# Performance work log

Measured on AMD Instinct MI355X. Metric: run time of the kernel, lower is better.

Reference implementation:

```python
import jax, jax.numpy as jnp
import numpy as np

NG, G = 256, 32          # num groups, pedestrians per group
E, H, MID, BN_EPS = 64, 64, 512, 1e-5
BOT = 32

def _bn(x, gamma, beta):
    # training-mode BatchNorm1d applied PER GROUP (axis=1 are the rows of
    # that group's pairwise batch), biased variance, eps=1e-5
    mean = jnp.mean(x, axis=1, keepdims=True)
    var = jnp.mean((x - mean) ** 2, axis=1, keepdims=True)
    return gamma * (x - mean) * jax.lax.rsqrt(var + BN_EPS) + beta

def setup_inputs() -> dict:
    key = jax.random.key(0)
    ks = jax.random.split(key, 8)
    B = NG * G
    starts = np.arange(NG, dtype=np.int64) * G
    seq_start_end = jnp.asarray(np.stack([starts, starts + G], axis=1))
    def lin(k, fi, fo):
        kw, kb = jax.random.split(k)
        lim = 1.0 / np.sqrt(fi)
        return (jax.random.uniform(kw, (fi, fo), jnp.float32, -lim, lim),
                jax.random.uniform(kb, (fo,), jnp.float32, -lim, lim))
    W_spatial, b_spatial = lin(ks[0], 2, E)
    W1, b1 = lin(ks[1], E + H, MID)
    W2, b2 = lin(ks[2], MID, BOT)
    return {
        'h_states': jax.random.normal(ks[3], (1, B, H), jnp.float32),
        'seq_start_end': seq_start_end,
        'end_pos': jax.random.normal(ks[4], (B, 2), jnp.float32),
        'W_spatial': W_spatial, 'b_spatial': b_spatial,
        'W1': W1, 'b1': b1,
        'gamma1': jnp.ones((MID,), jnp.float32), 'beta1': jnp.zeros((MID,), jnp.float32),
        'W2': W2, 'b2': b2,
        'gamma2': jnp.ones((BOT,), jnp.float32), 'beta2': jnp.zeros((BOT,), jnp.float32),
    }

def reference(h_states, seq_start_end, end_pos, W_spatial, b_spatial,
              W1, b1, gamma1, beta1, W2, b2, gamma2, beta2):
    B = end_pos.shape[0]
    ng = seq_start_end.shape[0]
    g = B // ng  # equal-size groups -> fully vectorized
    h = h_states.reshape(B, H).reshape(ng, g, H)
    pos = end_pos.reshape(ng, g, 2)
    # rel[n, i, j] = pos[n, j] - pos[n, i]  (matches repeat/tile in torch code)
    rel = pos[:, None, :, :] - pos[:, :, None, :]            # (ng, g, g, 2)
    emb = rel @ W_spatial + b_spatial                         # (ng, g, g, E)
    hb = jnp.broadcast_to(h[:, None, :, :], (ng, g, g, H))    # hidden of ped j
    x = jnp.concatenate([emb, hb], axis=-1).reshape(ng, g * g, E + H)
    x = jax.nn.relu(_bn(x @ W1 + b1, gamma1, beta1))          # (ng, g*g, 512)
    x = jax.nn.relu(_bn(x @ W2 + b2, gamma2, beta2))          # (ng, g*g, 32)
    pool = x.reshape(ng, g, g, BOT).max(axis=2)               # max over j
    return pool.reshape(B, BOT)
```

## Files before the change

### kernel.cpp

```cpp
#include <hip/hip_runtime.h>

#define GRP 32
#define HD 64
#define MIDD 512
#define LDSTR 520

typedef _Float16 half8 __attribute__((ext_vector_type(8)));
typedef float floatx4 __attribute__((ext_vector_type(4)));

__device__ inline half8 relu8(half8 x) {
    return __builtin_elementwise_max(x, (half8)(_Float16)0);
}

__launch_bounds__(512, 2)
__global__ void pool_all(const float* __restrict__ h_states,
                         const float* __restrict__ end_pos,
                         const float* __restrict__ Ws,
                         const float* __restrict__ W1,
                         const float* __restrict__ gamma1,
                         const float* __restrict__ beta1,
                         const float* __restrict__ W2,
                         const float* __restrict__ gamma2,
                         const float* __restrict__ beta2,
                         float* __restrict__ out) {
    __shared__ _Float16 Ash[32][LDSTR];
    __shared__ _Float16 Bsh[32][LDSTR];
    __shared__ _Float16 w2T[32][LDSTR];
    __shared__ float posx[32], posy[32];
    __shared__ float wr0s[512], wr1s[512];
    __shared__ float red[8][2][16][2];
    __shared__ float bns[32], bno[32];

    const int tid  = threadIdx.x;
    const int wave = tid >> 6;
    const int lane = tid & 63;
    const int quad = lane >> 4;
    const int n16  = lane & 15;
    const int g0   = blockIdx.x * GRP;

    if (tid < 32) {
        posx[tid] = end_pos[(g0 + tid) * 2];
        posy[tid] = end_pos[(g0 + tid) * 2 + 1];
    }

    half8 afr[2][2];
#pragma unroll
    for (int mt = 0; mt < 2; ++mt)
#pragma unroll
        for (int kk = 0; kk < 2; ++kk) {
            const float4* hp = (const float4*)(h_states + (size_t)(g0 + mt * 16 + n16) * HD + kk * 32 + quad * 8);
            float4 p0 = hp[0], p1 = hp[1];
            half8 a;
            a[0] = (_Float16)p0.x; a[1] = (_Float16)p0.y; a[2] = (_Float16)p0.z; a[3] = (_Float16)p0.w;
            a[4] = (_Float16)p1.x; a[5] = (_Float16)p1.y; a[6] = (_Float16)p1.z; a[7] = (_Float16)p1.w;
            afr[mt][kk] = a;
        }

    {
        const int c = tid;
        float p0[4] = {0.f, 0.f, 0.f, 0.f}, p1[4] = {0.f, 0.f, 0.f, 0.f};
#pragma unroll
        for (int e = 0; e < 64; e += 4) {
#pragma unroll
            for (int u = 0; u < 4; ++u) {
                float w = W1[(e + u) * MIDD + c];
                p0[u] = fmaf(Ws[e + u], w, p0[u]);
                p1[u] = fmaf(Ws[64 + e + u], w, p1[u]);
            }
        }
        wr0s[c] = (p0[0] + p0[1]) + (p0[2] + p0[3]);
        wr1s[c] = (p1[0] + p1[1]) + (p1[2] + p1[3]);
    }

    {
        const float4* W2v = (const float4*)W2;
#pragma unroll
        for (int it = 0; it < 8; ++it) {
            int i4 = tid + it * 512;
            float4 p = W2v[i4];
            int k = i4 >> 3, nn = (i4 & 7) * 4;
            w2T[nn][k]     = (_Float16)p.x;
            w2T[nn + 1][k] = (_Float16)p.y;
            w2T[nn + 2][k] = (_Float16)p.z;
            w2T[nn + 3][k] = (_Float16)p.w;
        }
    }

    floatx4 acc[2][4];
#pragma unroll
    for (int a = 0; a < 2; ++a)
#pragma unroll
        for (int b = 0; b < 4; ++b) acc[a][b] = (floatx4){0.f, 0.f, 0.f, 0.f};

    half8 bfr[4][2];
#pragma unroll
    for (int nt4 = 0; nt4 < 4; ++nt4) {
        const int c = (wave * 4 + nt4) * 16 + n16;
#pragma unroll
        for (int kk = 0; kk < 2; ++kk) {
            float t[8];
#pragma unroll
            for (int x = 0; x < 8; ++x) {
                int k = kk * 32 + quad * 8 + x;
                t[x] = W1[(size_t)(64 + k) * MIDD + c];
            }
            half8 b;
#pragma unroll
            for (int x = 0; x < 8; ++x) b[x] = (_Float16)t[x];
            bfr[nt4][kk] = b;
        }
    }
#pragma unroll
    for (int nt4 = 0; nt4 < 4; ++nt4)
#pragma unroll
        for (int kk = 0; kk < 2; ++kk)
#pragma unroll
            for (int mt = 0; mt < 2; ++mt)
                acc[mt][nt4] = __builtin_amdgcn_mfma_f32_16x16x32_f16(afr[mt][kk], bfr[nt4][kk], acc[mt][nt4], 0, 0, 0);

    __syncthreads();

#pragma unroll
    for (int nt4 = 0; nt4 < 4; ++nt4) {
        const int c = (wave * 4 + nt4) * 16 + n16;
        const float w0 = wr0s[c], w1 = wr1s[c];

        float su = 0.f, ssu = 0.f;
#pragma unroll
        for (int mt = 0; mt < 2; ++mt)
#pragma unroll
            for (int r = 0; r < 4; ++r) {
                int j = mt * 16 + quad * 4 + r;
                float u = acc[mt][nt4][r] + posx[j] * w0 + posy[j] * w1;
                acc[mt][nt4][r] = u;
                su += u;
                ssu = fmaf(u, u, ssu);
            }
        su  += __shfl_xor(su, 16);  su  += __shfl_xor(su, 32);
        ssu += __shfl_xor(ssu, 16); ssu += __shfl_xor(ssu, 32);

        float vv[8];
        float sv = 0.f, ssv = 0.f;
#pragma unroll
        for (int ii = 0; ii < 8; ++ii) {
            int i = quad * 8 + ii;
            float v = posx[i] * w0 + posy[i] * w1;
            vv[ii] = v;
            sv += v;
            ssv = fmaf(v, v, ssv);
        }
        sv  += __shfl_xor(sv, 16);  sv  += __shfl_xor(sv, 32);
        ssv += __shfl_xor(ssv, 16); ssv += __shfl_xor(ssv, 32);

        const float muu = su * (1.f / 32.f), muv = sv * (1.f / 32.f);
        const float var = (ssu * (1.f / 32.f) - muu * muu) + (ssv * (1.f / 32.f) - muv * muv);
        const float s    = gamma1[c] * rsqrtf(var + 1e-5f);
        const float boff = s * (muu - muv) - beta1[c];

#pragma unroll
        for (int mt = 0; mt < 2; ++mt)
#pragma unroll
            for (int r = 0; r < 4; ++r) {
                int j = mt * 16 + quad * 4 + r;
                Ash[j][c] = (_Float16)(s * acc[mt][nt4][r]);
            }
#pragma unroll
        for (int ii = 0; ii < 8; ++ii)
            Bsh[quad * 8 + ii][c] = (_Float16)fmaf(s, vv[ii], boff);
    }
    __syncthreads();

    floatx4 acc2[8][2];
#pragma unroll
    for (int a = 0; a < 8; ++a)
#pragma unroll
        for (int b = 0; b < 2; ++b) acc2[a][b] = (floatx4){0.f, 0.f, 0.f, 0.f};

    const int ib = wave * 4;
    half8 pa0[2], pa1[2], pw0[2], pw1[2], pbf[2][4];
    {
        const int kb = quad * 8;
        pw0[0] = *(const half8*)&w2T[n16][kb];
        pw1[0] = *(const half8*)&w2T[16 + n16][kb];
        pa0[0] = *(const half8*)&Ash[n16][kb];
        pa1[0] = *(const half8*)&Ash[16 + n16][kb];
#pragma unroll
        for (int mp = 0; mp < 4; ++mp) pbf[0][mp] = *(const half8*)&Bsh[ib + mp][kb];
    }
#pragma unroll
    for (int kk = 0; kk < 15; ++kk) {
        const int cur = kk & 1, nxt = cur ^ 1;
        {
            const int kb = (kk + 1) * 32 + quad * 8;
            pw0[nxt] = *(const half8*)&w2T[n16][kb];
            pw1[nxt] = *(const half8*)&w2T[16 + n16][kb];
            pa0[nxt] = *(const half8*)&Ash[n16][kb];
            pa1[nxt] = *(const half8*)&Ash[16 + n16][kb];
#pragma unroll
            for (int mp = 0; mp < 4; ++mp) pbf[nxt][mp] = *(const half8*)&Bsh[ib + mp][kb];
        }
#pragma unroll
        for (int mp = 0; mp < 4; ++mp) {
            const half8 bf = pbf[cur][mp];
            const half8 z0 = relu8(pa0[cur] - bf);
            const half8 z1 = relu8(pa1[cur] - bf);
            acc2[2 * mp][0]     = __builtin_amdgcn_mfma_f32_16x16x32_f16(z0, pw0[cur], acc2[2 * mp][0], 0, 0, 0);
            acc2[2 * mp][1]     = __builtin_amdgcn_mfma_f32_16x16x32_f16(z0, pw1[cur], acc2[2 * mp][1], 0, 0, 0);
            acc2[2 * mp + 1][0] = __builtin_amdgcn_mfma_f32_16x16x32_f16(z1, pw0[cur], acc2[2 * mp + 1][0], 0, 0, 0);
            acc2[2 * mp + 1][1] = __builtin_amdgcn_mfma_f32_16x16x32_f16(z1, pw1[cur], acc2[2 * mp + 1][1], 0, 0, 0);
        }
    }
    {
#pragma unroll
        for (int mp = 0; mp < 4; ++mp) {
            const half8 bf = pbf[1][mp];
            const half8 z0 = relu8(pa0[1] - bf);
            const half8 z1 = relu8(pa1[1] - bf);
            acc2[2 * mp][0]     = __builtin_amdgcn_mfma_f32_16x16x32_f16(z0, pw0[1], acc2[2 * mp][0], 0, 0, 0);
            acc2[2 * mp][1]     = __builtin_amdgcn_mfma_f32_16x16x32_f16(z0, pw1[1], acc2[2 * mp][1], 0, 0, 0);
            acc2[2 * mp + 1][0] = __builtin_amdgcn_mfma_f32_16x16x32_f16(z1, pw0[1], acc2[2 * mp + 1][0], 0, 0, 0);
            acc2[2 * mp + 1][1] = __builtin_amdgcn_mfma_f32_16x16x32_f16(z1, pw1[1], acc2[2 * mp + 1][1], 0, 0, 0);
        }
    }

    float s0 = 0.f, q0 = 0.f, s1 = 0.f, q1 = 0.f;
#pragma unroll
    for (int mt = 0; mt < 8; ++mt)
#pragma unroll
        for (int r = 0; r < 4; ++r) {
            float v0 = acc2[mt][0][r], v1 = acc2[mt][1][r];
            s0 += v0; q0 = fmaf(v0, v0, q0);
            s1 += v1; q1 = fmaf(v1, v1, q1);
        }
    s0 += __shfl_xor(s0, 16); s0 += __shfl_xor(s0, 32);
    q0 += __shfl_xor(q0, 16); q0 += __shfl_xor(q0, 32);
    s1 += __shfl_xor(s1, 16); s1 += __shfl_xor(s1, 32);
    q1 += __shfl_xor(q1, 16); q1 += __shfl_xor(q1, 32);
    if (lane < 16) {
        red[wave][0][lane][0] = s0; red[wave][0][lane][1] = q0;
        red[wave][1][lane][0] = s1; red[wave][1][lane][1] = q1;
    }
    __syncthreads();
    if (tid < 32) {
        const int nt = tid >> 4, n = tid & 15;
        float s = 0.f, q = 0.f;
#pragma unroll
        for (int w = 0; w < 8; ++w) { s += red[w][nt][n][0]; q += red[w][nt][n][1]; }
        const float mu  = s * (1.f / 1024.f);
        const float var = q * (1.f / 1024.f) - mu * mu;
        const float sc  = gamma2[tid] * rsqrtf(var + 1e-5f);
        bns[tid] = sc;
        bno[tid] = beta2[tid] - sc * mu;
    }
    __syncthreads();

#pragma unroll
    for (int nt = 0; nt < 2; ++nt) {
        const int c = nt * 16 + n16;
        const float sc = bns[c], off = bno[c];
#pragma unroll
        for (int a = 0; a < 4; ++a) {
            float m = 0.f;
#pragma unroll
            for (int p = 0; p < 2; ++p)
#pragma unroll
                for (int r = 0; r < 4; ++r)
                    m = fmaxf(m, fmaf(sc, acc2[2 * a + p][nt][r], off));
            m = fmaxf(m, __shfl_xor(m, 16));
            m = fmaxf(m, __shfl_xor(m, 32));
            if (quad == nt) {
                const int i = wave * 4 + a;
                out[(size_t)(g0 + i) * 32 + c] = m;
            }
        }
    }
}

extern "C" void kernel_launch(void* const* d_in, const int* in_sizes, int n_in,
                              void* d_out, int out_size, void* d_ws, size_t ws_size,
                              hipStream_t stream) {
    (void)in_sizes; (void)n_in; (void)out_size; (void)d_ws; (void)ws_size;
    const float* h_states  = (const float*)d_in[0];
    const float* end_pos   = (const float*)d_in[2];
    const float* W_spatial = (const float*)d_in[3];
    const float* W1        = (const float*)d_in[5];
    const float* gamma1    = (const float*)d_in[7];
    const float* beta1     = (const float*)d_in[8];
    const float* W2        = (const float*)d_in[9];
    const float* gamma2    = (const float*)d_in[11];
    const float* beta2     = (const float*)d_in[12];
    float* out = (float*)d_out;

    pool_all<<<dim3(256), dim3(512), 0, stream>>>(h_states, end_pos, W_spatial, W1,
                                                  gamma1, beta1, W2, gamma2, beta2, out);
}
```

Baseline: 96.51 us.

## Precompute fp16 weight fragments in a prep kernel and drop per-block W2 LDS staging

Adds a small prep kernel that computes the spatial-projected W1 rows and packs W1 (hidden part) and W2 into fp16 MFMA fragment order in workspace. The main kernel then loads the B fragments directly with vector loads instead of strided fp32 gathers and conversions, and reads W2 fragments from global memory instead of transposing W2 into LDS. This removes redundant per-block weight preprocessing and cuts LDS use, at the cost of an extra kernel launch and global loads inside the second GEMM loop.

```diff
diff --git a/kernel.cpp b/kernel.cpp
--- a/kernel.cpp
+++ b/kernel.cpp
@@ -5,6 +5,9 @@
 #define MIDD 512
 #define LDSTR 520
 
+#define WS_W1B_OFF 4096
+#define WS_W2_OFF  (4096 + 65536)
+
 typedef _Float16 half8 __attribute__((ext_vector_type(8)));
 typedef float floatx4 __attribute__((ext_vector_type(4)));
 
@@ -12,22 +15,68 @@
     return __builtin_elementwise_max(x, (half8)(_Float16)0);
 }
 
+__launch_bounds__(512)
+__global__ void prep(const float* __restrict__ Ws,
+                     const float* __restrict__ W1,
+                     const float* __restrict__ W2,
+                     float* __restrict__ wsf) {
+    const int b = blockIdx.x, t = threadIdx.x;
+    _Float16* w1b = (_Float16*)((char*)wsf + WS_W1B_OFF);
+    _Float16* w2f = (_Float16*)((char*)wsf + WS_W2_OFF);
+    if (b == 0) {
+        const int c = t;
+        float p0[4] = {0.f, 0.f, 0.f, 0.f}, p1[4] = {0.f, 0.f, 0.f, 0.f};
+#pragma unroll
+        for (int e = 0; e < 64; e += 4) {
+#pragma unroll
+            for (int u = 0; u < 4; ++u) {
+                float w = W1[(e + u) * MIDD + c];
+                p0[u] = fmaf(Ws[e + u], w, p0[u]);
+                p1[u] = fmaf(Ws[64 + e + u], w, p1[u]);
+            }
+        }
+        wsf[c]       = (p0[0] + p0[1]) + (p0[2] + p0[3]);
+        wsf[512 + c] = (p1[0] + p1[1]) + (p1[2] + p1[3]);
+    } else if (b <= 8) {
+        const int base = (b - 1) * 4096 + t * 8;
+        const int fid = base >> 3;
+        const int n16 = fid & 15, quad = (fid >> 4) & 3;
+        const int kk = (fid >> 6) & 1, cblk = fid >> 7;
+        const int c = cblk * 16 + n16;
+#pragma unroll
+        for (int x = 0; x < 8; ++x) {
+            int k = kk * 32 + quad * 8 + x;
+            w1b[base + x] = (_Float16)W1[(size_t)(64 + k) * MIDD + c];
+        }
+    } else {
+        const int base0 = (b - 9) * 8192 + t * 16;
+#pragma unroll
+        for (int i = 0; i < 16; i += 8) {
+            const int base = base0 + i;
+            const int fid = base >> 3;
+            const int n16 = fid & 15, quad = (fid >> 4) & 3;
+            const int kk = (fid >> 6) & 15, nt = (fid >> 10) & 1;
+#pragma unroll
+            for (int x = 0; x < 8; ++x) {
+                int k = kk * 32 + quad * 8 + x;
+                w2f[base + x] = (_Float16)W2[(size_t)k * 32 + nt * 16 + n16];
+            }
+        }
+    }
+}
+
 __launch_bounds__(512, 2)
 __global__ void pool_all(const float* __restrict__ h_states,
                          const float* __restrict__ end_pos,
-                         const float* __restrict__ Ws,
-                         const float* __restrict__ W1,
+                         const float* __restrict__ wsf,
                          const float* __restrict__ gamma1,
                          const float* __restrict__ beta1,
-                         const float* __restrict__ W2,
                          const float* __restrict__ gamma2,
                          const float* __restrict__ beta2,
                          float* __restrict__ out) {
     __shared__ _Float16 Ash[32][LDSTR];
     __shared__ _Float16 Bsh[32][LDSTR];
-    __shared__ _Float16 w2T[32][LDSTR];
     __shared__ float posx[32], posy[32];
-    __shared__ float wr0s[512], wr1s[512];
     __shared__ float red[8][2][16][2];
     __shared__ float bns[32], bno[32];
 
@@ -37,6 +86,9 @@
     const int quad = lane >> 4;
     const int n16  = lane & 15;
     const int g0   = blockIdx.x * GRP;
+
+    const _Float16* w1bf = (const _Float16*)((const char*)wsf + WS_W1B_OFF);
+    const _Float16* w2f  = (const _Float16*)((const char*)wsf + WS_W2_OFF);
 
     if (tid < 32) {
         posx[tid] = end_pos[(g0 + tid) * 2];
@@ -56,60 +108,28 @@
             afr[mt][kk] = a;
         }
 
-    {
-        const int c = tid;
-        float p0[4] = {0.f, 0.f, 0.f, 0.f}, p1[4] = {0.f, 0.f, 0.f, 0.f};
-#pragma unroll
-        for (int e = 0; e < 64; e += 4) {
-#pragma unroll
-            for (int u = 0; u < 4; ++u) {
-                float w = W1[(e + u) * MIDD + c];
-                p0[u] = fmaf(Ws[e + u], w, p0[u]);
-                p1[u] = fmaf(Ws[64 + e + u], w, p1[u]);
-            }
-        }
-        wr0s[c] = (p0[0] + p0[1]) + (p0[2] + p0[3]);
-        wr1s[c] = (p1[0] + p1[1]) + (p1[2] + p1[3]);
-    }
-
-    {
-        const float4* W2v = (const float4*)W2;
-#pragma unroll
-        for (int it = 0; it < 8; ++it) {
-            int i4 = tid + it * 512;
-            float4 p = W2v[i4];
-            int k = i4 >> 3, nn = (i4 & 7) * 4;
-            w2T[nn][k]     = (_Float16)p.x;
-            w2T[nn + 1][k] = (_Float16)p.y;
-            w2T[nn + 2][k] = (_Float16)p.z;
-            w2T[nn + 3][k] = (_Float16)p.w;
-        }
-    }
-
-    floatx4 acc[2][4];
-#pragma unroll
-    for (int a = 0; a < 2; ++a)
-#pragma unroll
-        for (int b = 0; b < 4; ++b) acc[a][b] = (floatx4){0.f, 0.f, 0.f, 0.f};
-
     half8 bfr[4][2];
+#pragma unroll
+    for (int nt4 = 0; nt4 < 4; ++nt4)
+#pragma unroll
+        for (int kk = 0; kk < 2; ++kk)
+            bfr[nt4][kk] = *(const half8*)&w1bf[(size_t)((((wave * 4 + nt4) * 2 + kk) * 4 + quad) * 16 + n16) * 8];
+
+    float wr0[4], wr1[4], g1v[4], b1v[4];
 #pragma unroll
     for (int nt4 = 0; nt4 < 4; ++nt4) {
         const int c = (wave * 4 + nt4) * 16 + n16;
-#pragma unroll
-        for (int kk = 0; kk < 2; ++kk) {
-            float t[8];
-#pragma unroll
-            for (int x = 0; x < 8; ++x) {
-                int k = kk * 32 + quad * 8 + x;
-                t[x] = W1[(size_t)(64 + k) * MIDD + c];
-            }
-            half8 b;
-#pragma unroll
-            for (int x = 0; x < 8; ++x) b[x] = (_Float16)t[x];
-            bfr[nt4][kk] = b;
-        }
-    }
+        wr0[nt4] = wsf[c];
+        wr1[nt4] = wsf[512 + c];
+        g1v[nt4] = gamma1[c];
+        b1v[nt4] = beta1[c];
+    }
+
+    floatx4 acc[2][4];
+#pragma unroll
+    for (int a = 0; a < 2; ++a)
+#pragma unroll
+        for (int b = 0; b < 4; ++b) acc[a][b] = (floatx4){0.f, 0.f, 0.f, 0.f};
 #pragma unroll
     for (int nt4 = 0; nt4 < 4; ++nt4)
 #pragma unroll
@@ -123,7 +143,7 @@
 #pragma unroll
     for (int nt4 = 0; nt4 < 4; ++nt4) {
         const int c = (wave * 4 + nt4) * 16 + n16;
-        const float w0 = wr0s[c], w1 = wr1s[c];
+        const float w0 = wr0[nt4], w1 = wr1[nt4];
 
         float su = 0.f, ssu = 0.f;
 #pragma unroll
@@ -154,8 +174,8 @@
 
         const float muu = su * (1.f / 32.f), muv = sv * (1.f / 32.f);
         const float var = (ssu * (1.f / 32.f) - muu * muu) + (ssv * (1.f / 32.f) - muv * muv);
-        const float s    = gamma1[c] * rsqrtf(var + 1e-5f);
-        const float boff = s * (muu - muv) - beta1[c];
+        const float s    = g1v[nt4] * rsqrtf(var + 1e-5f);
+        const float boff = s * (muu - muv) - b1v[nt4];
 
 #pragma unroll
         for (int mt = 0; mt < 2; ++mt)
@@ -168,6 +188,11 @@
         for (int ii = 0; ii < 8; ++ii)
             Bsh[quad * 8 + ii][c] = (_Float16)fmaf(s, vv[ii], boff);
     }
+
+    half8 pw0[2], pw1[2];
+    pw0[0] = *(const half8*)&w2f[(size_t)(((0 * 16 + 0) * 4 + quad) * 16 + n16) * 8];
+    pw1[0] = *(const half8*)&w2f[(size_t)(((1 * 16 + 0) * 4 + quad) * 16 + n16) * 8];
+
     __syncthreads();
 
     floatx4 acc2[8][2];
@@ -177,11 +202,9 @@
         for (int b = 0; b < 2; ++b) acc2[a][b] = (floatx4){0.f, 0.f, 0.f, 0.f};
 
     const int ib = wave * 4;
-    half8 pa0[2], pa1[2], pw0[2], pw1[2], pbf[2][4];
+    half8 pa0[2], pa1[2], pbf[2][4];
     {
         const int kb = quad * 8;
-        pw0[0] = *(const half8*)&w2T[n16][kb];
-        pw1[0] = *(const half8*)&w2T[16 + n16][kb];
         pa0[0] = *(const half8*)&Ash[n16][kb];
         pa1[0] = *(const half8*)&Ash[16 + n16][kb];
 #pragma unroll
@@ -192,8 +215,8 @@
         const int cur = kk & 1, nxt = cur ^ 1;
         {
             const int kb = (kk + 1) * 32 + quad * 8;
-            pw0[nxt] = *(const half8*)&w2T[n16][kb];
-            pw1[nxt] = *(const half8*)&w2T[16 + n16][kb];
+            pw0[nxt] = *(const half8*)&w2f[(size_t)((((kk + 1)) * 4 + quad) * 16 + n16) * 8];
+            pw1[nxt] = *(const half8*)&w2f[(size_t)(((16 + kk + 1) * 4 + quad) * 16 + n16) * 8];
             pa0[nxt] = *(const half8*)&Ash[n16][kb];
             pa1[nxt] = *(const half8*)&Ash[16 + n16][kb];
 #pragma unroll
@@ -279,7 +302,7 @@
 extern "C" void kernel_launch(void* const* d_in, const int* in_sizes, int n_in,
                               void* d_out, int out_size, void* d_ws, size_t ws_size,
                               hipStream_t stream) {
-    (void)in_sizes; (void)n_in; (void)out_size; (void)d_ws; (void)ws_size;
+    (void)in_sizes; (void)n_in; (void)out_size; (void)ws_size;
     const float* h_states  = (const float*)d_in[0];
     const float* end_pos   = (const float*)d_in[2];
     const float* W_spatial = (const float*)d_in[3];
@@ -290,7 +313,9 @@
     const float* gamma2    = (const float*)d_in[11];
     const float* beta2     = (const float*)d_in[12];
     float* out = (float*)d_out;
-
-    pool_all<<<dim3(256), dim3(512), 0, stream>>>(h_states, end_pos, W_spatial, W1,
-                                                  gamma1, beta1, W2, gamma2, beta2, out);
+    float* wsf = (float*)d_ws;
+
+    prep<<<dim3(11), dim3(512), 0, stream>>>(W_spatial, W1, W2, wsf);
+    pool_all<<<dim3(256), dim3(512), 0, stream>>>(h_states, end_pos, wsf,
+                                                  gamma1, beta1, gamma2, beta2, out);
 }
```

Measured after the change: 99.36 us. 1.03x slower.
